# Optimization experiments

Hardware: AMD Instinct MI355X
Metric: run time of the kernel (lower is better)

The kernel has to match this reference:

```python
import jax, jax.numpy as jnp
import numpy as np

N = 50000      # nodes
E = 800000     # edges
D_IN = 128     # embedding_in
EP = 200000    # prediction edge pairs
CONV_DIMS = [D_IN, 128, 64, 32]
LIN_DIMS = [32, 16, 8, 1]


def setup_inputs() -> dict:
    key = jax.random.key(0)
    ks = jax.random.split(key, 20)
    inp = {
        "x": jax.random.normal(ks[0], (N, D_IN), dtype=jnp.float32),
        "edge_index": jax.random.randint(ks[1], (2, E), 0, N, dtype=jnp.int64 if jax.config.jax_enable_x64 else jnp.int32),
        "pred_edges": jax.random.randint(ks[2], (EP, 2), 0, N, dtype=jnp.int64 if jax.config.jax_enable_x64 else jnp.int32),
    }
    k = 3
    for i in range(3):  # GCNConv weights [in,out] + bias (torch GCNConv has bias)
        din, dout = CONV_DIMS[i], CONV_DIMS[i + 1]
        inp[f"cw{i}"] = jax.random.normal(ks[k], (din, dout), dtype=jnp.float32) / np.sqrt(din); k += 1
        inp[f"cb{i}"] = jax.random.normal(ks[k], (dout,), dtype=jnp.float32) * 0.01; k += 1
    for i in range(3):  # Linear weights stored [in,out]
        din, dout = LIN_DIMS[i], LIN_DIMS[i + 1]
        inp[f"lw{i}"] = jax.random.normal(ks[k], (din, dout), dtype=jnp.float32) / np.sqrt(din); k += 1
        inp[f"lb{i}"] = jax.random.normal(ks[k], (dout,), dtype=jnp.float32) * 0.01; k += 1
    return inp


def gcn_conv(x, W, b, src, dst, n):
    """PyG GCNConv: D^-1/2 (A + I) D^-1/2 X W + b, deg over dst incl. self-loop."""
    h = x @ W  # [n, dout]
    deg = jax.ops.segment_sum(jnp.ones_like(dst, dtype=h.dtype), dst, num_segments=n) + 1.0
    dis = jax.lax.rsqrt(deg)  # deg >= 1 (self loop)
    msg = h[src] * (dis[src] * dis[dst])[:, None]      # gather + per-edge normalize
    out = jax.ops.segment_sum(msg, dst, num_segments=n)  # scatter-add into targets
    out = out + h * (dis * dis)[:, None]                # self-loop contribution
    return out + b


def reference(x, edge_index, pred_edges, cw0, cb0, cw1, cb1, cw2, cb2,
              lw0, lb0, lw1, lb1, lw2, lb2):
    src, dst = edge_index[0], edge_index[1]
    n = x.shape[0]
    for W, b in ((cw0, cb0), (cw1, cb1), (cw2, cb2)):
        x = jax.nn.relu(gcn_conv(x, W, b, src, dst, n))
    x = jax.nn.relu(x @ lw0 + lb0)
    x = jax.nn.relu(x @ lw1 + lb1)
    x = jax.nn.sigmoid(x @ lw2 + lb2)  # [n, 1]
    s = x[:, 0]
    # x[pred_edges] -> [EP,2,1]; mul of pair, transpose+flatten -> [EP]
    return s[pred_edges[:, 0]] * s[pred_edges[:, 1]]
```

## Files before the change

kernel.cpp:

```cpp
#include <hip/hip_runtime.h>
#include <math.h>

constexpr int NN  = 50000;
constexpr int NP  = 50048;
constexpr int NE  = 800000;
constexpr int NEP = 200000;

constexpr int NBKT  = 256;
constexpr int CAP   = 4096;
constexpr int CAPC  = 4096;
constexpr int CHUNK = 4096;

constexpr int BKB = (NE + CHUNK - 1) / CHUNK;
constexpr int W0B = 128 * 128 / 256;
constexpr int W1B = 128 * 64 / 256;
constexpr int W2B = 64 * 32 / 256;
constexpr int FRONT_BLOCKS = BKB + W0B + W1B + W2B;

constexpr int GEMM0_BLKS = NP / 64;
constexpr int NODE_BLKS32 = (NN + 31) / 32;

constexpr float M0_SCALE  = 16.0f;
constexpr float M0_ISCALE = 1.0f / 16.0f;
constexpr float M1_SCALE  = 16.0f;
constexpr float M1_ISCALE = 1.0f / 16.0f;
constexpr float M2_SCALE  = 16.0f;
constexpr float M2_ISCALE = 1.0f / 16.0f;

typedef _Float16 half8_t  __attribute__((ext_vector_type(8)));
typedef __fp16   fp16x2_t __attribute__((ext_vector_type(2)));
typedef float    float4_t __attribute__((ext_vector_type(4)));

static inline int cdiv(long long a, int b) { return (int)((a + b - 1) / b); }

static __device__ inline unsigned char f32_to_fp8(float v) {
    int p = __builtin_amdgcn_cvt_pk_fp8_f32(v, v, 0, false);
    return (unsigned char)(p & 0xFF);
}

static __device__ inline void fp8x8_acc(uint2 u, float d, float* a) {
    auto f0 = __builtin_amdgcn_cvt_pk_f32_fp8((int)u.x, false);
    auto f1 = __builtin_amdgcn_cvt_pk_f32_fp8((int)u.x, true);
    auto f2 = __builtin_amdgcn_cvt_pk_f32_fp8((int)u.y, false);
    auto f3 = __builtin_amdgcn_cvt_pk_f32_fp8((int)u.y, true);
    a[0] = fmaf(f0[0], d, a[0]); a[1] = fmaf(f0[1], d, a[1]);
    a[2] = fmaf(f1[0], d, a[2]); a[3] = fmaf(f1[1], d, a[3]);
    a[4] = fmaf(f2[0], d, a[4]); a[5] = fmaf(f2[1], d, a[5]);
    a[6] = fmaf(f3[0], d, a[6]); a[7] = fmaf(f3[1], d, a[7]);
}

static __device__ inline void fp8x16_acc(uint4 u, float d, float* a) {
    fp8x8_acc((uint2){u.x, u.y}, d, a);
    fp8x8_acc((uint2){u.z, u.w}, d, a + 8);
}

static __device__ inline void fp8x8_add(uint2 u, float* a) {
    auto f0 = __builtin_amdgcn_cvt_pk_f32_fp8((int)u.x, false);
    auto f1 = __builtin_amdgcn_cvt_pk_f32_fp8((int)u.x, true);
    auto f2 = __builtin_amdgcn_cvt_pk_f32_fp8((int)u.y, false);
    auto f3 = __builtin_amdgcn_cvt_pk_f32_fp8((int)u.y, true);
    a[0] += f0[0]; a[1] += f0[1];
    a[2] += f1[0]; a[3] += f1[1];
    a[4] += f2[0]; a[5] += f2[1];
    a[6] += f3[0]; a[7] += f3[1];
}

__global__ __launch_bounds__(256) void k_front(const int* __restrict__ src,
        const int* __restrict__ dst, int* __restrict__ binCnt,
        unsigned int* __restrict__ ebuf,
        const float* __restrict__ cw0, _Float16* __restrict__ WT0,
        const float* __restrict__ cw1, _Float16* __restrict__ WT1,
        const float* __restrict__ cw2, _Float16* __restrict__ WT2) {
    const int tid = threadIdx.x;
    const int bid = blockIdx.x;

    if (bid < BKB) {
        __shared__ int hist[NBKT];
        __shared__ int base[NBKT];
        __shared__ int cur[NBKT];
        const int e0 = bid * CHUNK;
        hist[tid] = 0;
        __syncthreads();
        int  s[16], bn[16], dl[16];
        bool okq[4];
#pragma unroll
        for (int q = 0; q < 4; ++q) {
            int i = e0 + q * 1024 + tid * 4;
            bool ok = i < NE;
            okq[q] = ok;
            if (ok) {
                int4 d4 = *(const int4*)(dst + i);
                int4 s4 = *(const int4*)(src + i);
                s[q*4+0] = s4.x; bn[q*4+0] = d4.x >> 8; dl[q*4+0] = d4.x & 255;
                s[q*4+1] = s4.y; bn[q*4+1] = d4.y >> 8; dl[q*4+1] = d4.y & 255;
                s[q*4+2] = s4.z; bn[q*4+2] = d4.z >> 8; dl[q*4+2] = d4.z & 255;
                s[q*4+3] = s4.w; bn[q*4+3] = d4.w >> 8; dl[q*4+3] = d4.w & 255;
                atomicAdd(&hist[bn[q*4+0]], 1);
                atomicAdd(&hist[bn[q*4+1]], 1);
                atomicAdd(&hist[bn[q*4+2]], 1);
                atomicAdd(&hist[bn[q*4+3]], 1);
            }
        }
        __syncthreads();
        base[tid] = hist[tid] ? atomicAdd(&binCnt[tid], hist[tid]) : 0;
        cur[tid] = 0;
        __syncthreads();
#pragma unroll
        for (int q = 0; q < 4; ++q) {
            if (okq[q]) {
#pragma unroll
                for (int u = 0; u < 4; ++u) {
                    int j = q * 4 + u;
                    int slot = base[bn[j]] + atomicAdd(&cur[bn[j]], 1);
                    ebuf[bn[j] * CAP + slot] = (unsigned int)s[j] | ((unsigned int)dl[j] << 16);
                }
            }
        }
        return;
    }
    if (bid < BKB + W0B) {
        int idx = (bid - BKB) * 256 + tid;
        int k = idx >> 7, n = idx & 127;
        WT0[(size_t)n * 128 + k] = (_Float16)cw0[idx];
        return;
    }
    if (bid < BKB + W0B + W1B) {
        int idx = (bid - BKB - W0B) * 256 + tid;
        int k = idx >> 6, n = idx & 63;
        WT1[(size_t)n * 128 + k] = (_Float16)cw1[idx];
        return;
    }
    {
        int idx = (bid - BKB - W0B - W1B) * 256 + tid;
        int k = idx >> 5, n = idx & 31;
        WT2[(size_t)n * 64 + k] = (_Float16)cw2[idx];
    }
}

__global__ __launch_bounds__(256) void k_csr_gemm0(const unsigned int* __restrict__ ebuf,
        const int* __restrict__ binCnt, int* __restrict__ off, float* __restrict__ dis,
        unsigned short* __restrict__ csr,
        const float* __restrict__ X, const _Float16* __restrict__ WT,
        unsigned char* __restrict__ g, int n) {
    const int tid = threadIdx.x;
    const int bid = blockIdx.x;

    if (bid < NBKT) {
        __shared__ int hist[256];
        __shared__ int sh[256];
        __shared__ int cur[256];
        const int bin = bid;
        const int cnt = binCnt[bin];
        const unsigned int* eb = ebuf + (size_t)bin * CAP;

        hist[tid] = 0;
        __syncthreads();
        for (int i = tid; i < cnt; i += 256)
            atomicAdd(&hist[eb[i] >> 16], 1);
        __syncthreads();

        int v  = hist[tid];
        int pv = (v + 3) & ~3;
        sh[tid] = pv;
        __syncthreads();
        for (int d = 1; d < 256; d <<= 1) {
            int t = (tid >= d) ? sh[tid - d] : 0;
            __syncthreads();
            sh[tid] += t;
            __syncthreads();
        }
        int start = bin * CAPC + (sh[tid] - pv);

        int node = bin * 256 + tid;
        if (node < NN) {
            off[node] = start | (pv << 20);
            dis[node] = rsqrtf((float)v + 1.0f);
        } else if (node == NN) {
            dis[node] = 0.f;
        }
        cur[tid] = start;
        __syncthreads();

        for (int i = tid; i < cnt; i += 256) {
            unsigned int e = eb[i];
            int p = atomicAdd(&cur[e >> 16], 1);
            csr[p] = (unsigned short)(e & 0xFFFFu);
        }
        for (int k2 = v; k2 < pv; ++k2) csr[start + k2] = (unsigned short)NN;
        return;
    }

    constexpr int K = 128, DOUT = 128;
    constexpr int NC = 64, NT = 4, KT = 4, MT = 2;

    const int gb   = bid - NBKT;
    const int L    = tid & 63;
    const int w    = tid >> 6;
    const int wc   = w & 1;
    const int wr   = w >> 1;
    const int r0   = gb * 64 + wr * 32;
    const int c0   = wc * NC;
    const int quad = L >> 4;
    const int lm   = L & 15;

    float4_t acc[MT][NT];
#pragma unroll
    for (int mt = 0; mt < MT; ++mt)
#pragma unroll
        for (int nt = 0; nt < NT; ++nt) acc[mt][nt] = (float4_t){0.f, 0.f, 0.f, 0.f};

#pragma unroll
    for (int kt = 0; kt < KT; ++kt) {
        half8_t a[MT], b[NT];
#pragma unroll
        for (int mt = 0; mt < MT; ++mt) {
            const float* xr = X + (size_t)(r0 + mt * 16 + lm) * K + kt * 32 + quad * 8;
            float4 u = *(const float4*)xr;
            float4 v = *(const float4*)(xr + 4);
            union { fp16x2_t h2[4]; half8_t h8; } cv;
            cv.h2[0] = __builtin_amdgcn_cvt_pkrtz(u.x, u.y);
            cv.h2[1] = __builtin_amdgcn_cvt_pkrtz(u.z, u.w);
            cv.h2[2] = __builtin_amdgcn_cvt_pkrtz(v.x, v.y);
            cv.h2[3] = __builtin_amdgcn_cvt_pkrtz(v.z, v.w);
            a[mt] = cv.h8;
        }
#pragma unroll
        for (int nt = 0; nt < NT; ++nt)
            b[nt] = *(const half8_t*)(WT + (size_t)(c0 + nt * 16 + lm) * K + kt * 32 + quad * 8);
#pragma unroll
        for (int mt = 0; mt < MT; ++mt)
#pragma unroll
            for (int nt = 0; nt < NT; ++nt)
                acc[mt][nt] = __builtin_amdgcn_mfma_f32_16x16x32_f16(a[mt], b[nt], acc[mt][nt], 0, 0, 0);
    }

#pragma unroll
    for (int mt = 0; mt < MT; ++mt) {
        int rb = r0 + mt * 16 + quad * 4;
#pragma unroll
        for (int nt = 0; nt < NT; ++nt) {
            int c = c0 + nt * 16 + lm;
#pragma unroll
            for (int reg = 0; reg < 4; ++reg) {
                int r = rb + reg;
                if (r < n)       g[(size_t)r * DOUT + c] = f32_to_fp8(acc[mt][nt][reg] * M0_SCALE);
                else if (r == n) g[(size_t)r * DOUT + c] = 0;
            }
        }
    }
}

__global__ __launch_bounds__(256) void k_agg_gemm16(const unsigned char* __restrict__ gin,
        const float* __restrict__ dis, const float* __restrict__ bias,
        const int* __restrict__ off, const unsigned short* __restrict__ csr,
        const _Float16* __restrict__ WT, unsigned char* __restrict__ gout, int n) {
    constexpr int DIN = 128, DOUT = 64;
    constexpr int XS = DIN + 8;
    __shared__ _Float16 sX[32 * XS];

    const int tid  = threadIdx.x;
    const int l8   = tid & 7;
    const int ln   = tid >> 3;
    const int r0   = blockIdx.x * 32;
    const int node = r0 + ln;

    const uint4* gp = (const uint4*)gin;

    if (blockIdx.x == 0 && tid < DOUT / 8)
        ((uint2*)(gout + (size_t)n * DOUT))[tid] = (uint2){0u, 0u};

    if (node < n) {
        float dd = dis[node];
        uint4 hv = gp[(size_t)node * 8 + l8];
        float a[16] = {0.f,0.f,0.f,0.f,0.f,0.f,0.f,0.f,0.f,0.f,0.f,0.f,0.f,0.f,0.f,0.f};
        fp8x16_acc(hv, dd, a);

        int pk = off[node];
        int e0 = pk & 0xFFFFF;
        int e1 = e0 + (pk >> 20);
        int e = e0;
        for (; e + 7 < e1; e += 8) {
            ushort4 c4 = *(const ushort4*)(csr + e);
            ushort4 c8 = *(const ushort4*)(csr + e + 4);
            uint4 v0 = gp[(size_t)c4.x * 8 + l8];
            uint4 v1 = gp[(size_t)c4.y * 8 + l8];
            uint4 v2 = gp[(size_t)c4.z * 8 + l8];
            uint4 v3 = gp[(size_t)c4.w * 8 + l8];
            uint4 v4 = gp[(size_t)c8.x * 8 + l8];
            uint4 v5 = gp[(size_t)c8.y * 8 + l8];
            uint4 v6 = gp[(size_t)c8.z * 8 + l8];
            uint4 v7 = gp[(size_t)c8.w * 8 + l8];
            float d0 = dis[c4.x], d1 = dis[c4.y], d2 = dis[c4.z], d3 = dis[c4.w];
            float d4 = dis[c8.x], d5 = dis[c8.y], d6 = dis[c8.z], d7 = dis[c8.w];
            fp8x16_acc(v0, d0, a); fp8x16_acc(v1, d1, a);
            fp8x16_acc(v2, d2, a); fp8x16_acc(v3, d3, a);
            fp8x16_acc(v4, d4, a); fp8x16_acc(v5, d5, a);
            fp8x16_acc(v6, d6, a); fp8x16_acc(v7, d7, a);
        }
        if (e < e1) {
            ushort4 c4 = *(const ushort4*)(csr + e);
            uint4 v0 = gp[(size_t)c4.x * 8 + l8];
            uint4 v1 = gp[(size_t)c4.y * 8 + l8];
            uint4 v2 = gp[(size_t)c4.z * 8 + l8];
            uint4 v3 = gp[(size_t)c4.w * 8 + l8];
            float d0 = dis[c4.x], d1 = dis[c4.y], d2 = dis[c4.z], d3 = dis[c4.w];
            fp8x16_acc(v0, d0, a); fp8x16_acc(v1, d1, a);
            fp8x16_acc(v2, d2, a); fp8x16_acc(v3, d3, a);
        }
        float ddp = dd * M0_ISCALE;
        half8_t o0, o1;
#pragma unroll
        for (int j = 0; j < 8; ++j) {
            o0[j] = (_Float16)fmaxf(fmaf(a[j],     ddp, bias[l8 * 16 + j]),     0.f);
            o1[j] = (_Float16)fmaxf(fmaf(a[j + 8], ddp, bias[l8 * 16 + 8 + j]), 0.f);
        }
        *(half8_t*)(sX + ln * XS + l8 * 16)     = o0;
        *(half8_t*)(sX + ln * XS + l8 * 16 + 8) = o1;
    } else {
        half8_t z = (half8_t){(_Float16)0.f,(_Float16)0.f,(_Float16)0.f,(_Float16)0.f,
                              (_Float16)0.f,(_Float16)0.f,(_Float16)0.f,(_Float16)0.f};
        *(half8_t*)(sX + ln * XS + l8 * 16)     = z;
        *(half8_t*)(sX + ln * XS + l8 * 16 + 8) = z;
    }
    __syncthreads();

    const int L    = tid & 63;
    const int w    = tid >> 6;
    const int quad = L >> 4;
    const int lm   = L & 15;
    const int c0   = w * 16;

#pragma unroll
    for (int mh = 0; mh < 2; ++mh) {
        const int m0 = mh * 16;
        float4_t acc = (float4_t){0.f, 0.f, 0.f, 0.f};
#pragma unroll
        for (int kt = 0; kt < DIN / 32; ++kt) {
            half8_t b  = *(const half8_t*)(WT + (size_t)(c0 + lm) * DIN + kt * 32 + quad * 8);
            half8_t aF = *(const half8_t*)(sX + (m0 + lm) * XS + kt * 32 + quad * 8);
            acc = __builtin_amdgcn_mfma_f32_16x16x32_f16(aF, b, acc, 0, 0, 0);
        }
        int rb = r0 + m0 + quad * 4;
        float dv[4];
        *(float4*)dv = *(const float4*)(dis + rb);
#pragma unroll
        for (int reg = 0; reg < 4; ++reg) {
            int r = rb + reg;
            if (r < n) gout[(size_t)r * DOUT + c0 + lm] = f32_to_fp8(acc[reg] * dv[reg] * M1_SCALE);
        }
    }
}

__global__ __launch_bounds__(256) void k_agg_gemm8(const unsigned char* __restrict__ gin,
        const float* __restrict__ dis, const float* __restrict__ bias,
        const int* __restrict__ off, const unsigned short* __restrict__ csr,
        const _Float16* __restrict__ WT, unsigned char* __restrict__ gout, int n) {
    constexpr int DIN = 64, DOUT = 32;
    constexpr int XS = DIN + 8;
    __shared__ _Float16 sX[32 * XS];

    const int tid  = threadIdx.x;
    const int l8   = tid & 7;
    const int ln   = tid >> 3;
    const int r0   = blockIdx.x * 32;
    const int node = r0 + ln;

    const uint2* gp = (const uint2*)gin;

    if (node < n) {
        float dd = dis[node];
        uint2 hv = gp[(size_t)node * 8 + l8];
        float a[8] = {0.f, 0.f, 0.f, 0.f, 0.f, 0.f, 0.f, 0.f};
        fp8x8_add(hv, a);
        int pk = off[node];
        int e0 = pk & 0xFFFFF;
        int e1 = e0 + (pk >> 20);
        int e = e0;
        for (; e + 7 < e1; e += 8) {
            ushort4 c4 = *(const ushort4*)(csr + e);
            ushort4 c8 = *(const ushort4*)(csr + e + 4);
            uint2 v0 = gp[(size_t)c4.x * 8 + l8];
            uint2 v1 = gp[(size_t)c4.y * 8 + l8];
            uint2 v2 = gp[(size_t)c4.z * 8 + l8];
            uint2 v3 = gp[(size_t)c4.w * 8 + l8];
            uint2 v4 = gp[(size_t)c8.x * 8 + l8];
            uint2 v5 = gp[(size_t)c8.y * 8 + l8];
            uint2 v6 = gp[(size_t)c8.z * 8 + l8];
            uint2 v7 = gp[(size_t)c8.w * 8 + l8];
            fp8x8_add(v0, a); fp8x8_add(v1, a);
            fp8x8_add(v2, a); fp8x8_add(v3, a);
            fp8x8_add(v4, a); fp8x8_add(v5, a);
            fp8x8_add(v6, a); fp8x8_add(v7, a);
        }
        if (e < e1) {
            ushort4 c4 = *(const ushort4*)(csr + e);
            uint2 v0 = gp[(size_t)c4.x * 8 + l8];
            uint2 v1 = gp[(size_t)c4.y * 8 + l8];
            uint2 v2 = gp[(size_t)c4.z * 8 + l8];
            uint2 v3 = gp[(size_t)c4.w * 8 + l8];
            fp8x8_add(v0, a); fp8x8_add(v1, a);
            fp8x8_add(v2, a); fp8x8_add(v3, a);
        }
        float ddp = dd * M1_ISCALE;
        half8_t o;
#pragma unroll
        for (int j = 0; j < 8; ++j)
            o[j] = (_Float16)fmaxf(fmaf(a[j], ddp, bias[l8 * 8 + j]), 0.f);
        *(half8_t*)(sX + ln * XS + l8 * 8) = o;
    } else {
        *(half8_t*)(sX + ln * XS + l8 * 8) =
            (half8_t){(_Float16)0.f, (_Float16)0.f, (_Float16)0.f, (_Float16)0.f,
                      (_Float16)0.f, (_Float16)0.f, (_Float16)0.f, (_Float16)0.f};
    }
    __syncthreads();

    const int L    = tid & 63;
    const int w    = tid >> 6;
    const int quad = L >> 4;
    const int lm   = L & 15;
    const int c0   = (w & 1) * 16;
    const int m0   = (w >> 1) * 16;

    float4_t acc = (float4_t){0.f, 0.f, 0.f, 0.f};
#pragma unroll
    for (int kt = 0; kt < DIN / 32; ++kt) {
        half8_t b  = *(const half8_t*)(WT + (size_t)(c0 + lm) * DIN + kt * 32 + quad * 8);
        half8_t aF = *(const half8_t*)(sX + (m0 + lm) * XS + kt * 32 + quad * 8);
        acc = __builtin_amdgcn_mfma_f32_16x16x32_f16(aF, b, acc, 0, 0, 0);
    }
    int rb = r0 + m0 + quad * 4;
    float dv[4];
    *(float4*)dv = *(const float4*)(dis + rb);
#pragma unroll
    for (int reg = 0; reg < 4; ++reg) {
        int r = rb + reg;
        if (r < n)       gout[(size_t)r * DOUT + c0 + lm] = f32_to_fp8(acc[reg] * dv[reg] * M2_SCALE);
        else if (r == n) gout[(size_t)r * DOUT + c0 + lm] = 0;
    }
}

__global__ __launch_bounds__(256) void k_agg_mlp(const unsigned char* __restrict__ g,
        const float* __restrict__ dis, const float* __restrict__ b,
        const int* __restrict__ off, const unsigned short* __restrict__ csr,
        const float* __restrict__ lw0, const float* __restrict__ lb0,
        const float* __restrict__ lw1, const float* __restrict__ lb1,
        const float* __restrict__ lw2, const float* __restrict__ lb2,
        float* __restrict__ sv, int n) {
    __shared__ float sh[32 * 33];
    const int tid  = threadIdx.x;
    const int l8   = tid & 7;
    const int lane = l8 & 3;
    const int grp  = l8 >> 2;
    const int ln   = tid >> 3;
    const int node = blockIdx.x * 32 + ln;

    const uint2* gp = (const uint2*)g;

    if (node < n) {
        float dd = dis[node];
        float a[8] = {0.f, 0.f, 0.f, 0.f, 0.f, 0.f, 0.f, 0.f};
        if (grp == 0) fp8x8_add(gp[(size_t)node * 4 + lane], a);
        int pk = off[node];
        int e0 = pk & 0xFFFFF;
        int e1 = e0 + (pk >> 20);
        for (int e = e0 + grp * 4; e < e1; e += 8) {
            ushort4 c4 = *(const ushort4*)(csr + e);
            uint2 v0 = gp[(size_t)c4.x * 4 + lane];
            uint2 v1 = gp[(size_t)c4.y * 4 + lane];
            uint2 v2 = gp[(size_t)c4.z * 4 + lane];
            uint2 v3 = gp[(size_t)c4.w * 4 + lane];
            fp8x8_add(v0, a); fp8x8_add(v1, a);
            fp8x8_add(v2, a); fp8x8_add(v3, a);
        }
#pragma unroll
        for (int j = 0; j < 8; ++j) a[j] += __shfl_xor(a[j], 4);
        if (grp == 0) {
            float ddp = dd * M2_ISCALE;
            float* row = sh + ln * 33 + lane * 8;
#pragma unroll
            for (int j = 0; j < 8; ++j)
                row[j] = fmaxf(fmaf(a[j], ddp, b[lane * 8 + j]), 0.f);
        }
    }
    __syncthreads();

    if (tid < 32) {
        int node2 = blockIdx.x * 32 + tid;
        if (node2 < n) {
            const float* v = sh + tid * 33;
            float a[16];
#pragma unroll
            for (int j = 0; j < 16; ++j) {
                float acc = lb0[j];
#pragma unroll
                for (int k = 0; k < 32; ++k) acc = fmaf(v[k], lw0[k * 16 + j], acc);
                a[j] = fmaxf(acc, 0.f);
            }
            float b8[8];
#pragma unroll
            for (int j = 0; j < 8; ++j) {
                float acc = lb1[j];
#pragma unroll
                for (int k = 0; k < 16; ++k) acc = fmaf(a[k], lw1[k * 8 + j], acc);
                b8[j] = fmaxf(acc, 0.f);
            }
            float z = lb2[0];
#pragma unroll
            for (int k = 0; k < 8; ++k) z = fmaf(b8[k], lw2[k], z);
            sv[node2] = 1.0f / (1.0f + expf(-z));
        }
    }
}

__global__ void k_pred(const float* __restrict__ s, const int* __restrict__ pe,
                       float* __restrict__ out, int ep2) {
    int i = blockIdx.x * blockDim.x + threadIdx.x;
    if (i >= ep2) return;
    int4 p = ((const int4*)pe)[i];
    float2 o;
    o.x = s[p.x] * s[p.y];
    o.y = s[p.z] * s[p.w];
    ((float2*)out)[i] = o;
}

extern "C" void kernel_launch(void* const* d_in, const int* in_sizes, int n_in,
                              void* d_out, int out_size, void* d_ws, size_t ws_size,
                              hipStream_t stream) {
    const float* x   = (const float*)d_in[0];
    const int*   ei  = (const int*)d_in[1];
    const int*   pe  = (const int*)d_in[2];
    const float* cw0 = (const float*)d_in[3];
    const float* cb0 = (const float*)d_in[4];
    const float* cw1 = (const float*)d_in[5];
    const float* cb1 = (const float*)d_in[6];
    const float* cw2 = (const float*)d_in[7];
    const float* cb2 = (const float*)d_in[8];
    const float* lw0 = (const float*)d_in[9];
    const float* lb0 = (const float*)d_in[10];
    const float* lw1 = (const float*)d_in[11];
    const float* lb1 = (const float*)d_in[12];
    const float* lw2 = (const float*)d_in[13];
    const float* lb2 = (const float*)d_in[14];

    const int* src = ei;
    const int* dst = ei + NE;

    char* w = (char*)d_ws;
    float*          dis  = (float*)w;           w += sizeof(float) * (NN + 16);
    unsigned char*  M0   = (unsigned char*)w;   w += (size_t)(NN + 1) * 128;
    unsigned char*  M1   = (unsigned char*)w;   w += (size_t)(NN + 1) * 64;
    unsigned char*  M2   = (unsigned char*)w;   w += (size_t)(NN + 1) * 32;
    float*          sv   = (float*)w;           w += sizeof(float) * NN;
    _Float16*       WT0  = (_Float16*)w;        w += sizeof(_Float16) * 128 * 128;
    _Float16*       WT1  = (_Float16*)w;        w += sizeof(_Float16) * 64 * 128;
    _Float16*       WT2  = (_Float16*)w;        w += sizeof(_Float16) * 32 * 64;
    int*            off  = (int*)w;             w += sizeof(int) * NN;
    unsigned short* csr  = (unsigned short*)w;  w += sizeof(unsigned short) * (size_t)NBKT * CAPC;
    int*            binCnt = (int*)w;           w += sizeof(int) * NBKT;
    unsigned int*   ebuf = (unsigned int*)w;    w += sizeof(unsigned int) * (size_t)NBKT * CAP;

    const int T = 256;

    (void)hipMemsetAsync(binCnt, 0, sizeof(int) * NBKT, stream);
    k_front<<<FRONT_BLOCKS, 256, 0, stream>>>(src, dst, binCnt, ebuf,
                                              cw0, WT0, cw1, WT1, cw2, WT2);

    k_csr_gemm0<<<NBKT + GEMM0_BLKS, 256, 0, stream>>>(ebuf, binCnt, off, dis, csr,
                                                       x, WT0, M0, NN);

    k_agg_gemm16<<<NODE_BLKS32, 256, 0, stream>>>(M0, dis, cb0,
                                                  off, csr, WT1, M1, NN);

    k_agg_gemm8<<<NODE_BLKS32, 256, 0, stream>>>(M1, dis, cb1,
                                                 off, csr, WT2, M2, NN);

    k_agg_mlp<<<NODE_BLKS32, 256, 0, stream>>>(M2, dis, cb2, off, csr,
                                               lw0, lb0, lw1, lb1, lw2, lb2, sv, NN);

    k_pred<<<cdiv(NEP / 2, T), T, 0, stream>>>(sv, pe, (float*)d_out, NEP / 2);
}
```

Measured before the change: 182.6 us.

## Sort nodes by degree within buckets to balance aggregation work per block

During CSR construction each 256-node bucket bitonic-sorts its nodes by padded degree and writes a permutation. The three aggregation kernels then process nodes in that permuted order, so the 32 nodes handled together in a block (and the 8 per wavefront) have similar edge counts and less lane divergence in the gather loops. The cost is an extra sort in the CSR kernel, extra shared-memory permutation loads, scattered output writes, and per-row dis loads in place of a single vector load.

```diff
diff --git a/kernel.cpp b/kernel.cpp
--- a/kernel.cpp
+++ b/kernel.cpp
@@ -139,7 +139,7 @@
 
 __global__ __launch_bounds__(256) void k_csr_gemm0(const unsigned int* __restrict__ ebuf,
         const int* __restrict__ binCnt, int* __restrict__ off, float* __restrict__ dis,
-        unsigned short* __restrict__ csr,
+        unsigned short* __restrict__ csr, unsigned short* __restrict__ perm,
         const float* __restrict__ X, const _Float16* __restrict__ WT,
         unsigned char* __restrict__ g, int n) {
     const int tid = threadIdx.x;
@@ -149,6 +149,7 @@
         __shared__ int hist[256];
         __shared__ int sh[256];
         __shared__ int cur[256];
+        __shared__ int key[256];
         const int bin = bid;
         const int cnt = binCnt[bin];
         const unsigned int* eb = ebuf + (size_t)bin * CAP;
@@ -179,6 +180,7 @@
             dis[node] = 0.f;
         }
         cur[tid] = start;
+        key[tid] = (node < NN) ? ((pv << 8) | tid) : -1;
         __syncthreads();
 
         for (int i = tid; i < cnt; i += 256) {
@@ -187,6 +189,22 @@
             csr[p] = (unsigned short)(e & 0xFFFFu);
         }
         for (int k2 = v; k2 < pv; ++k2) csr[start + k2] = (unsigned short)NN;
+
+        for (int k = 2; k <= 256; k <<= 1) {
+            for (int j = k >> 1; j > 0; j >>= 1) {
+                __syncthreads();
+                int ixj = tid ^ j;
+                if (ixj > tid) {
+                    int a = key[tid], b = key[ixj];
+                    bool desc = ((tid & k) == 0);
+                    if (desc ? (a < b) : (a > b)) { key[tid] = b; key[ixj] = a; }
+                }
+            }
+        }
+        __syncthreads();
+        perm[bin * 256 + tid] = (key[tid] >= 0)
+            ? (unsigned short)(bin * 256 + (key[tid] & 255))
+            : (unsigned short)NN;
         return;
     }
 
@@ -253,16 +271,21 @@
 __global__ __launch_bounds__(256) void k_agg_gemm16(const unsigned char* __restrict__ gin,
         const float* __restrict__ dis, const float* __restrict__ bias,
         const int* __restrict__ off, const unsigned short* __restrict__ csr,
+        const unsigned short* __restrict__ perm,
         const _Float16* __restrict__ WT, unsigned char* __restrict__ gout, int n) {
     constexpr int DIN = 128, DOUT = 64;
     constexpr int XS = DIN + 8;
     __shared__ _Float16 sX[32 * XS];
-
-    const int tid  = threadIdx.x;
-    const int l8   = tid & 7;
-    const int ln   = tid >> 3;
-    const int r0   = blockIdx.x * 32;
-    const int node = r0 + ln;
+    __shared__ unsigned short permS[32];
+
+    const int tid = threadIdx.x;
+    const int l8  = tid & 7;
+    const int ln  = tid >> 3;
+    const int r0  = blockIdx.x * 32;
+
+    if (tid < 32) permS[tid] = perm[r0 + tid];
+    __syncthreads();
+    const int node = permS[ln];
 
     const uint4* gp = (const uint4*)gin;
 
@@ -340,13 +363,12 @@
             half8_t aF = *(const half8_t*)(sX + (m0 + lm) * XS + kt * 32 + quad * 8);
             acc = __builtin_amdgcn_mfma_f32_16x16x32_f16(aF, b, acc, 0, 0, 0);
         }
-        int rb = r0 + m0 + quad * 4;
-        float dv[4];
-        *(float4*)dv = *(const float4*)(dis + rb);
+        int lb = m0 + quad * 4;
 #pragma unroll
         for (int reg = 0; reg < 4; ++reg) {
-            int r = rb + reg;
-            if (r < n) gout[(size_t)r * DOUT + c0 + lm] = f32_to_fp8(acc[reg] * dv[reg] * M1_SCALE);
+            int real = permS[lb + reg];
+            if (real < n)
+                gout[(size_t)real * DOUT + c0 + lm] = f32_to_fp8(acc[reg] * dis[real] * M1_SCALE);
         }
     }
 }
@@ -354,18 +376,26 @@
 __global__ __launch_bounds__(256) void k_agg_gemm8(const unsigned char* __restrict__ gin,
         const float* __restrict__ dis, const float* __restrict__ bias,
         const int* __restrict__ off, const unsigned short* __restrict__ csr,
+        const unsigned short* __restrict__ perm,
         const _Float16* __restrict__ WT, unsigned char* __restrict__ gout, int n) {
     constexpr int DIN = 64, DOUT = 32;
     constexpr int XS = DIN + 8;
     __shared__ _Float16 sX[32 * XS];
-
-    const int tid  = threadIdx.x;
-    const int l8   = tid & 7;
-    const int ln   = tid >> 3;
-    const int r0   = blockIdx.x * 32;
-    const int node = r0 + ln;
+    __shared__ unsigned short permS[32];
+
+    const int tid = threadIdx.x;
+    const int l8  = tid & 7;
+    const int ln  = tid >> 3;
+    const int r0  = blockIdx.x * 32;
+
+    if (tid < 32) permS[tid] = perm[r0 + tid];
+    __syncthreads();
+    const int node = permS[ln];
 
     const uint2* gp = (const uint2*)gin;
+
+    if (blockIdx.x == 0 && tid < DOUT / 8)
+        ((uint2*)(gout + (size_t)n * DOUT))[tid] = (uint2){0u, 0u};
 
     if (node < n) {
         float dd = dis[node];
@@ -428,31 +458,35 @@
         half8_t aF = *(const half8_t*)(sX + (m0 + lm) * XS + kt * 32 + quad * 8);
         acc = __builtin_amdgcn_mfma_f32_16x16x32_f16(aF, b, acc, 0, 0, 0);
     }
-    int rb = r0 + m0 + quad * 4;
-    float dv[4];
-    *(float4*)dv = *(const float4*)(dis + rb);
+    int lb = m0 + quad * 4;
 #pragma unroll
     for (int reg = 0; reg < 4; ++reg) {
-        int r = rb + reg;
-        if (r < n)       gout[(size_t)r * DOUT + c0 + lm] = f32_to_fp8(acc[reg] * dv[reg] * M2_SCALE);
-        else if (r == n) gout[(size_t)r * DOUT + c0 + lm] = 0;
+        int real = permS[lb + reg];
+        if (real < n)
+            gout[(size_t)real * DOUT + c0 + lm] = f32_to_fp8(acc[reg] * dis[real] * M2_SCALE);
     }
 }
 
 __global__ __launch_bounds__(256) void k_agg_mlp(const unsigned char* __restrict__ g,
         const float* __restrict__ dis, const float* __restrict__ b,
         const int* __restrict__ off, const unsigned short* __restrict__ csr,
+        const unsigned short* __restrict__ perm,
         const float* __restrict__ lw0, const float* __restrict__ lb0,
         const float* __restrict__ lw1, const float* __restrict__ lb1,
         const float* __restrict__ lw2, const float* __restrict__ lb2,
         float* __restrict__ sv, int n) {
     __shared__ float sh[32 * 33];
+    __shared__ unsigned short permS[32];
     const int tid  = threadIdx.x;
     const int l8   = tid & 7;
     const int lane = l8 & 3;
     const int grp  = l8 >> 2;
     const int ln   = tid >> 3;
-    const int node = blockIdx.x * 32 + ln;
+    const int r0   = blockIdx.x * 32;
+
+    if (tid < 32) permS[tid] = perm[r0 + tid];
+    __syncthreads();
+    const int node = permS[ln];
 
     const uint2* gp = (const uint2*)g;
 
@@ -485,7 +519,7 @@
     __syncthreads();
 
     if (tid < 32) {
-        int node2 = blockIdx.x * 32 + tid;
+        int node2 = permS[tid];
         if (node2 < n) {
             const float* v = sh + tid * 33;
             float a[16];
@@ -556,6 +590,7 @@
     _Float16*       WT2  = (_Float16*)w;        w += sizeof(_Float16) * 32 * 64;
     int*            off  = (int*)w;             w += sizeof(int) * NN;
     unsigned short* csr  = (unsigned short*)w;  w += sizeof(unsigned short) * (size_t)NBKT * CAPC;
+    unsigned short* perm = (unsigned short*)w;  w += sizeof(unsigned short) * 65536;
     int*            binCnt = (int*)w;           w += sizeof(int) * NBKT;
     unsigned int*   ebuf = (unsigned int*)w;    w += sizeof(unsigned int) * (size_t)NBKT * CAP;
 
@@ -566,15 +601,15 @@
                                               cw0, WT0, cw1, WT1, cw2, WT2);
 
     k_csr_gemm0<<<NBKT + GEMM0_BLKS, 256, 0, stream>>>(ebuf, binCnt, off, dis, csr,
-                                                       x, WT0, M0, NN);
+                                                       perm, x, WT0, M0, NN);
 
     k_agg_gemm16<<<NODE_BLKS32, 256, 0, stream>>>(M0, dis, cb0,
-                                                  off, csr, WT1, M1, NN);
+                                                  off, csr, perm, WT1, M1, NN);
 
     k_agg_gemm8<<<NODE_BLKS32, 256, 0, stream>>>(M1, dis, cb1,
-                                                 off, csr, WT2, M2, NN);
-
-    k_agg_mlp<<<NODE_BLKS32, 256, 0, stream>>>(M2, dis, cb2, off, csr,
+                                                 off, csr, perm, WT2, M2, NN);
+
+    k_agg_mlp<<<NODE_BLKS32, 256, 0, stream>>>(M2, dis, cb2, off, csr, perm,
                                                lw0, lb0, lw1, lb1, lw2, lb2, sv, NN);
 
     k_pred<<<cdiv(NEP / 2, T), T, 0, stream>>>(sv, pe, (float*)d_out, NEP / 2);
```

Measured after the change: 195.0 us. 1.07x slower.
